# Kernel optimization log

Hardware: AMD Instinct MI355X
Metric: run time of the kernel (lower is better)

The kernel has to match this reference:

```python
import jax, jax.numpy as jnp
import numpy as np

N_HEAD = 12


def setup_inputs() -> dict:
    key = jax.random.key(0)
    kx, kq, kk, kv = jax.random.split(key, 4)
    b, n, d = 2, 2048, 768
    x = jax.random.normal(kx, (b, n, d), dtype=jnp.float32)
    # nn.Linear weights stored as [d_out, d_in]; y = x @ W.T (no bias, qkv_bias=False)
    scale = 1.0 / np.sqrt(d)
    Wq = jax.random.normal(kq, (d, d), dtype=jnp.float32) * scale
    Wk = jax.random.normal(kk, (d, d), dtype=jnp.float32) * scale
    Wv = jax.random.normal(kv, (d, d), dtype=jnp.float32) * scale
    return {"x": x, "Wq": Wq, "Wk": Wk, "Wv": Wv}


def reference(x, Wq, Wk, Wv):
    b, n, d = x.shape
    h = N_HEAD
    hd = d // h
    # linear projections (bias=False): x @ W.T, then split heads -> [b, h, n, hd]
    q = (x @ Wq.T).reshape(b, n, h, hd).transpose(0, 2, 1, 3)
    k = (x @ Wk.T).reshape(b, n, h, hd).transpose(0, 2, 1, 3)
    v = (x @ Wv.T).reshape(b, n, h, hd).transpose(0, 2, 1, 3)
    # raw (unscaled!) attention scores, matching the source (no / sqrt(head_dim))
    scores = jnp.einsum('bhqd,bhkd->bhqk', q, k)  # [b, h, n, n]
    causal = jnp.tril(jnp.ones((n, n), dtype=bool))
    scores = jnp.where(causal, scores, -jnp.inf)
    weights = jax.nn.softmax(scores, axis=-1)
    out = jnp.einsum('bhqk,bhkd->bhqd', weights, v)  # [b, h, n, hd]
    return out.transpose(0, 2, 1, 3).reshape(b, n, d)
```

## Files before the change

### kernel.cpp

```cpp
#include <hip/hip_runtime.h>
#include <hip/hip_bf16.h>
#include <stdint.h>

#define Bsz 2
#define NT  2048
#define DM  768
#define NH  12
#define HD  64
#define MT  (Bsz * NT)
#define NCAT (3 * DM)

typedef float    f32x4  __attribute__((ext_vector_type(4)));
typedef float    f32x16 __attribute__((ext_vector_type(16)));
typedef short    s16x8  __attribute__((ext_vector_type(8)));
typedef _Float16 f16x8  __attribute__((ext_vector_type(8)));
typedef int      v2i    __attribute__((ext_vector_type(2)));

#define GLOBAL_AS __attribute__((address_space(1)))
#define SHARED_AS __attribute__((address_space(3)))
#define LOG2E 1.44269504088896f

__device__ inline unsigned short f2h(float f) {
    union { _Float16 h; unsigned short u; } c; c.h = (_Float16)f; return c.u;
}
__device__ inline f16x8 ldh(const short* p) {
    return __builtin_bit_cast(f16x8, *(const s16x8*)p);
}
__device__ inline float exp2i(float x) {
    float r;
    asm("v_exp_f32 %0, %1" : "=v"(r) : "v"(x));
    return r;
}
__device__ inline int cvtpkh(float lo, float hi_) {
    int r;
    asm("v_cvt_pkrtz_f16_f32 %0, %1, %2" : "=v"(r) : "v"(lo), "v"(hi_));
    return r;
}
__device__ inline void plswap(int& a, int& b) {
    v2i r = __builtin_amdgcn_permlane32_swap(a, b, false, false);
    a = r[0]; b = r[1];
}
__device__ inline f16x8 mk8(int a, int b, int c, int d) {
    union { int i[4]; f16x8 v; } u;
    u.i[0] = a; u.i[1] = b; u.i[2] = c; u.i[3] = d;
    return u.v;
}
#define mfma32 __builtin_amdgcn_mfma_f32_32x32x16_f16
#define mfma16 __builtin_amdgcn_mfma_f32_16x16x32_f16


__global__ __launch_bounds__(256) void cvt_x_kernel(const float* __restrict__ x,
                                                    short* __restrict__ xf, int n8) {
    int i = blockIdx.x * blockDim.x + threadIdx.x;
    if (i >= n8) return;
    const float4* p = (const float4*)x + (size_t)i * 2;
    float4 a = p[0], b = p[1];
    float v[8] = {a.x, a.y, a.z, a.w, b.x, b.y, b.z, b.w};
    union { unsigned short s[8]; uint4 q; } H;
#pragma unroll
    for (int j = 0; j < 8; ++j) H.s[j] = f2h(v[j]);
    ((uint4*)xf)[i] = H.q;
}

__global__ __launch_bounds__(256) void cvt_w_kernel(const float* __restrict__ Wq,
                                                    const float* __restrict__ Wk,
                                                    const float* __restrict__ Wv,
                                                    short* __restrict__ Wf, int per8) {
    int i = blockIdx.x * blockDim.x + threadIdx.x;
    if (i >= 3 * per8) return;
    const float* src; int j;
    if (i < per8)          { src = Wq; j = i; }
    else if (i < 2 * per8) { src = Wk; j = i - per8; }
    else                   { src = Wv; j = i - 2 * per8; }
    const float4* p = (const float4*)src + (size_t)j * 2;
    float4 a = p[0], b = p[1];
    float v[8] = {a.x, a.y, a.z, a.w, b.x, b.y, b.z, b.w};
    union { unsigned short s[8]; uint4 q; } H;
#pragma unroll
    for (int t = 0; t < 8; ++t) H.s[t] = f2h(v[t]);
    ((uint4*)Wf)[i] = H.q;
}


#define BM 128
#define BK 32
#define KSTEPS (DM / BK)

__global__ __launch_bounds__(256, 2) void qkv_proj_kernel(
        const short* __restrict__ xf, const short* __restrict__ Wf,
        short* __restrict__ Qf, short* __restrict__ Kf, short* __restrict__ Vf) {
    __shared__ short lds[2][2][BM * BK];

    const int tid = threadIdx.x;
    const int w = tid >> 6, lane = tid & 63;
    const int l15 = lane & 15, lg = lane >> 4;
    const int wr = w >> 1, wc = w & 1;

    const int tile_m = blockIdx.x * BM;
    const int tile_n = blockIdx.y * BM;

    const int arr = w >> 1, hlf = w & 1;
    const int srow = lane >> 2;
    const int scol = (lane & 3) * 8;
    const short* gsrc = (arr == 0) ? xf + (size_t)tile_m * DM
                                   : Wf + (size_t)tile_n * DM;
    const short* gsrc_lane = gsrc + (size_t)(hlf * 64 + srow) * DM + scol;

    f32x4 zero4 = {0.f, 0.f, 0.f, 0.f};
    f32x4 acc[4][4];
#pragma unroll
    for (int i = 0; i < 4; ++i)
#pragma unroll
        for (int j = 0; j < 4; ++j) acc[i][j] = zero4;

    auto stage = [&](int buf, int kt) {
        const short* g = gsrc_lane + kt * BK;
#pragma unroll
        for (int j = 0; j < 4; ++j) {
            __builtin_amdgcn_global_load_lds(
                (const GLOBAL_AS void*)(g + (size_t)j * 16 * DM),
                (SHARED_AS void*)(&lds[buf][arr][(hlf * 64 + j * 16) * BK]),
                16, 0, 0);
        }
    };

    stage(0, 0);
    int cur = 0;
    for (int kt = 0; kt < KSTEPS; ++kt) {
        __syncthreads();
        if (kt + 1 < KSTEPS) stage(cur ^ 1, kt + 1);

        f16x8 a[4], b[4];
#pragma unroll
        for (int f = 0; f < 4; ++f) {
            a[f] = ldh(&lds[cur][0][(wr * 64 + f * 16 + l15) * BK + lg * 8]);
            b[f] = ldh(&lds[cur][1][(wc * 64 + f * 16 + l15) * BK + lg * 8]);
        }
#pragma unroll
        for (int mf = 0; mf < 4; ++mf)
#pragma unroll
            for (int nf = 0; nf < 4; ++nf)
                acc[mf][nf] = mfma16(a[mf], b[nf], acc[mf][nf], 0, 0, 0);
        cur ^= 1;
    }

    const int zq = tile_n / DM;
    const int ncol0 = tile_n % DM;
#pragma unroll
    for (int mf = 0; mf < 4; ++mf) {
#pragma unroll
        for (int nf = 0; nf < 4; ++nf) {
            int col = ncol0 + wc * 64 + nf * 16 + l15;
            int h = col >> 6, dh = col & 63;
            int m0 = tile_m + wr * 64 + mf * 16 + lg * 4;
            int b2 = m0 >> 11, nt0 = m0 & (NT - 1);
            int bh_ = b2 * NH + h;
            if (zq == 2) {
                union { short s[4]; short4 v; } pk;
#pragma unroll
                for (int r = 0; r < 4; ++r) pk.s[r] = (short)f2h(acc[mf][nf][r]);
                *(short4*)&Vf[((size_t)bh_ * HD + dh) * NT + nt0] = pk.v;
            } else {
                short* Hp = (zq == 0) ? Qf : Kf;
                float scl = (zq == 0) ? LOG2E : 1.0f;
#pragma unroll
                for (int r = 0; r < 4; ++r) {
                    size_t oidx = ((size_t)bh_ * NT + nt0 + r) * HD + dh;
                    Hp[oidx] = (short)f2h(acc[mf][nf][r] * scl);
                }
            }
        }
    }
}


#define QB  128
#define KVB 64
#define NQB (NT / QB)
#define SEGT 8
#define SLOTS 40
#define OPA 600

__global__ __launch_bounds__(256) void attn_part_kernel(const short* __restrict__ Qf,
                                                        const short* __restrict__ Kf,
                                                        const short* __restrict__ Vf,
                                                        short* __restrict__ OpA_,
                                                        short* __restrict__ OpB_,
                                                        float2* __restrict__ ml) {
    const int s = blockIdx.x;
    int qb, seg;
    if (s < 4)       { qb = s;                  seg = 0; }
    else if (s < 12) { qb = 4 + ((s - 4) >> 1);   seg = (s - 4) & 1; }
    else if (s < 24) { qb = 8 + (s - 12) / 3;     seg = (s - 12) % 3; }
    else             { qb = 12 + ((s - 24) >> 2); seg = (s - 24) & 3; }
    const int bh = blockIdx.y;
    const int g = bh * SLOTS + s;
    const int tid = threadIdx.x;
    const int w = tid >> 6, lane = tid & 63;
    const int l31 = lane & 31, hi = lane >> 5;

    __shared__ __align__(16) short lds[2][2 * 4096];

    const size_t kvoff = (size_t)bh * NT * HD;
    const short* Kfb = Kf + kvoff;
    const short* Vb  = Vf + (size_t)bh * HD * NT;

    const short* sbase[4]; int sstr[4]; int sdof[4];
#pragma unroll
    for (int k = 0; k < 4; ++k) {
        int c = tid + 256 * k;
        int arr = c >> 9, idx = c & 511;
        int row = idx >> 3, ch = idx & 7;
        if (arr == 0) { sbase[k] = Kfb + (size_t)row * HD + ch * 8; sstr[k] = KVB * HD; }
        else          { sbase[k] = Vb + (size_t)row * NT + ch * 8;  sstr[k] = KVB; }
        sdof[k] = arr * 4096 + row * 64 + ((ch ^ (row & 7)) << 3);
    }

    const int q0w   = qb * QB + w * 32;
    const int qg    = q0w + l31;
    const int qmaxw = q0w + 31;

    f16x8 qf[4];
    const size_t qrow = kvoff + (size_t)qg * HD;
#pragma unroll
    for (int c = 0; c < 4; ++c) qf[c] = ldh(Qf + qrow + c * 16 + hi * 8);

    f32x16 o0{}, o1{};
    float m_run = -1e30f, l_run = 0.f;

    const int t0   = seg * SEGT;
    const int tend = min(t0 + SEGT, 2 * qb + 2);

    {
        uint4 ld0[4];
#pragma unroll
        for (int k = 0; k < 4; ++k) ld0[k] = *(const uint4*)(sbase[k] + (size_t)t0 * sstr[k]);
#pragma unroll
        for (int k = 0; k < 4; ++k) *(uint4*)(&lds[0][sdof[k]]) = ld0[k];
    }

    for (int t = t0; t < tend; ++t) {
        __syncthreads();
        const int cur = (t - t0) & 1;
        const int kv0 = t * KVB;
        const bool haveNext = (t + 1 < tend);
        uint4 ldn[4];
        if (haveNext) {
#pragma unroll
            for (int k = 0; k < 4; ++k)
                ldn[k] = *(const uint4*)(sbase[k] + (size_t)(t + 1) * sstr[k]);
        }

        if (kv0 <= qmaxw) {
            const short* Ks = &lds[cur][0];
            const short* Vs = &lds[cur][4096];
            f32x16 Sa{}, Sb{};
            const int swbA = l31 * 64;
            const int swbB = (32 + l31) * 64;
            const int sw7  = l31 & 7;
#pragma unroll
            for (int c = 0; c < 4; ++c) {
                int sh = (((c << 1) + hi) ^ sw7) << 3;
                Sa = mfma32(ldh(&Ks[swbA + sh]), qf[c], Sa, 0, 0, 0);
                Sb = mfma32(ldh(&Ks[swbB + sh]), qf[c], Sb, 0, 0, 0);
            }
            const bool haveB = (kv0 + 32 <= qmaxw);
            float pmax = -3e38f;
            if (kv0 + 31 > q0w) {
#pragma unroll
                for (int r = 0; r < 16; ++r) {
                    int kvg = kv0 + (r & 3) + 8 * (r >> 2) + 4 * hi;
                    Sa[r] = (kvg > qg) ? -3e38f : Sa[r];
                    pmax = fmaxf(pmax, Sa[r]);
                }
            } else {
#pragma unroll
                for (int r = 0; r < 16; ++r) pmax = fmaxf(pmax, Sa[r]);
            }
            if (haveB) {
                if (kv0 + 63 > q0w) {
#pragma unroll
                    for (int r = 0; r < 16; ++r) {
                        int kvg = kv0 + 32 + (r & 3) + 8 * (r >> 2) + 4 * hi;
                        Sb[r] = (kvg > qg) ? -3e38f : Sb[r];
                        pmax = fmaxf(pmax, Sb[r]);
                    }
                } else {
#pragma unroll
                    for (int r = 0; r < 16; ++r) pmax = fmaxf(pmax, Sb[r]);
                }
            }
            pmax = fmaxf(pmax, __shfl_xor(pmax, 32));
            if (!__all(pmax - m_run <= 11.5416f)) {
                float mn = fmaxf(m_run, pmax);
                float al = exp2i(m_run - mn);
                m_run = mn; l_run *= al;
                int ai = __builtin_bit_cast(int, al);
#pragma unroll
                for (int r = 0; r < 16; ++r) {
                    int kr = (r & 3) + 8 * (r >> 2) + 4 * hi;
                    float av = __builtin_bit_cast(float,
                                  __builtin_amdgcn_ds_bpermute(kr << 2, ai));
                    o0[r] *= av; o1[r] *= av;
                }
            }
            float rs = 0.f;
#pragma unroll
            for (int r = 0; r < 16; ++r) { Sa[r] = exp2i(Sa[r] - m_run); rs += Sa[r]; }
            if (haveB) {
#pragma unroll
                for (int r = 0; r < 16; ++r) { Sb[r] = exp2i(Sb[r] - m_run); rs += Sb[r]; }
            }
            rs += __shfl_xor(rs, 32);
            l_run += rs;
            {
                int cpk[8];
#pragma unroll
                for (int i = 0; i < 8; ++i) cpk[i] = cvtpkh(Sa[2 * i], Sa[2 * i + 1]);
                int a0 = cpk[0], b0 = cpk[2]; plswap(a0, b0);
                int a1 = cpk[1], b1 = cpk[3]; plswap(a1, b1);
                int a2 = cpk[4], b2 = cpk[6]; plswap(a2, b2);
                int a3 = cpk[5], b3 = cpk[7]; plswap(a3, b3);
                f16x8 pf[2] = { mk8(a0, a1, b0, b1), mk8(a2, a3, b2, b3) };
#pragma unroll
                for (int kc = 0; kc < 2; ++kc) {
                    int chunk = kc * 2 + hi;
                    int sh = (chunk ^ (l31 & 7)) << 3;
                    o0 = mfma32(pf[kc], ldh(&Vs[l31 * 64 + sh]), o0, 0, 0, 0);
                    o1 = mfma32(pf[kc], ldh(&Vs[(32 + l31) * 64 + sh]), o1, 0, 0, 0);
                }
            }
            if (haveB) {
                int cpk[8];
#pragma unroll
                for (int i = 0; i < 8; ++i) cpk[i] = cvtpkh(Sb[2 * i], Sb[2 * i + 1]);
                int a0 = cpk[0], b0 = cpk[2]; plswap(a0, b0);
                int a1 = cpk[1], b1 = cpk[3]; plswap(a1, b1);
                int a2 = cpk[4], b2 = cpk[6]; plswap(a2, b2);
                int a3 = cpk[5], b3 = cpk[7]; plswap(a3, b3);
                f16x8 pf[2] = { mk8(a0, a1, b0, b1), mk8(a2, a3, b2, b3) };
#pragma unroll
                for (int kc = 0; kc < 2; ++kc) {
                    int chunk = 4 + kc * 2 + hi;
                    int sh = (chunk ^ (l31 & 7)) << 3;
                    o0 = mfma32(pf[kc], ldh(&Vs[l31 * 64 + sh]), o0, 0, 0, 0);
                    o1 = mfma32(pf[kc], ldh(&Vs[(32 + l31) * 64 + sh]), o1, 0, 0, 0);
                }
            }
        }

        if (haveNext) {
#pragma unroll
            for (int k = 0; k < 4; ++k) *(uint4*)(&lds[cur ^ 1][sdof[k]]) = ldn[k];
        }
    }

    float inv = 1.0f / l_run;
    int ii = __builtin_bit_cast(int, inv);
    short* op = (g < OPA) ? OpA_ + (size_t)g * (QB * HD)
                          : OpB_ + (size_t)(g - OPA) * (QB * HD);
#pragma unroll
    for (int r = 0; r < 16; ++r) {
        int kr = (r & 3) + 8 * (r >> 2) + 4 * hi;
        float iv = __builtin_bit_cast(float, __builtin_amdgcn_ds_bpermute(kr << 2, ii));
        short* orow = op + (w * 32 + kr) * HD;
        orow[l31]      = (short)f2h(o0[r] * iv);
        orow[32 + l31] = (short)f2h(o1[r] * iv);
    }
    if (hi == 0) {
        float2 v; v.x = m_run; v.y = l_run;
        ml[(size_t)g * QB + w * 32 + l31] = v;
    }
}


__global__ __launch_bounds__(256) void combine_kernel(const short* __restrict__ OpA_,
                                                      const short* __restrict__ OpB_,
                                                      const float2* __restrict__ ml,
                                                      float* __restrict__ out) {
    const int qb = blockIdx.x, bh = blockIdx.y;
    const int b = bh / NH, h = bh % NH;
    const int nseg = (qb >> 2) + 1;
    const int baseg[4] = {0, 4, 12, 24};
    const int sbase = baseg[qb >> 2] + (qb & 3) * nseg;
    const int row = threadIdx.x >> 1;
    const int c0 = (threadIdx.x & 1) * 32;

    float m[4], l[4];
    float M = -3e38f;
    for (int s2 = 0; s2 < nseg; ++s2) {
        float2 t = ml[((size_t)(bh * SLOTS + sbase + s2)) * QB + row];
        m[s2] = t.x; l[s2] = t.y;
        M = fmaxf(M, t.x);
    }
    float wgt[4], L = 0.f;
    for (int s2 = 0; s2 < nseg; ++s2) {
        float e;
        asm("v_exp_f32 %0, %1" : "=v"(e) : "v"(m[s2] - M));
        wgt[s2] = l[s2] * e; L += wgt[s2];
    }
    float invL = 1.0f / L;

    float acc[32];
#pragma unroll
    for (int j = 0; j < 32; ++j) acc[j] = 0.f;
    for (int s2 = 0; s2 < nseg; ++s2) {
        int g = bh * SLOTS + sbase + s2;
        const short* opg = (g < OPA) ? OpA_ + (size_t)g * (QB * HD)
                                     : OpB_ + (size_t)(g - OPA) * (QB * HD);
        const short* oprow = opg + (size_t)row * HD + c0;
        float wg = wgt[s2] * invL;
#pragma unroll
        for (int v = 0; v < 4; ++v) {
            f16x8 d = ldh(oprow + v * 8);
#pragma unroll
            for (int j = 0; j < 8; ++j)
                acc[v * 8 + j] += wg * (float)d[j];
        }
    }
    float* orow = out + ((size_t)(b * NT + qb * QB + row)) * DM + h * HD + c0;
#pragma unroll
    for (int j = 0; j < 32; ++j) orow[j] = acc[j];
}


extern "C" void kernel_launch(void* const* d_in, const int* in_sizes, int n_in,
                              void* d_out, int out_size, void* d_ws, size_t ws_size,
                              hipStream_t stream) {
    const float* x  = (const float*)d_in[0];
    const float* Wq = (const float*)d_in[1];
    const float* Wk = (const float*)d_in[2];
    const float* Wv = (const float*)d_in[3];
    float* outp = (float*)d_out;

    const size_t MD = (size_t)MT * DM;
    const size_t DD = (size_t)DM * DM;

    short* wsp = (short*)d_ws;
    short* xf = wsp;
    short* Wf = xf + MD;
    short* Qf = Wf + 3 * DD;
    short* Kf = Qf + MD;
    short* Vf = Kf + MD;
    short* OpA_ = wsp;
    short* OpB_ = Vf + MD;
    float2* mlp = (float2*)(OpB_ + (size_t)360 * QB * HD);

    int n8x = (int)(MD / 8);
    cvt_x_kernel<<<dim3((n8x + 255) / 256), 256, 0, stream>>>(x, xf, n8x);
    int per8 = (int)(DD / 8);
    cvt_w_kernel<<<dim3((3 * per8 + 255) / 256), 256, 0, stream>>>(Wq, Wk, Wv, Wf, per8);
    qkv_proj_kernel<<<dim3(MT / BM, NCAT / BM), 256, 0, stream>>>(xf, Wf, Qf, Kf, Vf);
    attn_part_kernel<<<dim3(SLOTS, Bsz * NH), 256, 0, stream>>>(Qf, Kf, Vf, OpA_, OpB_, mlp);
    combine_kernel<<<dim3(NQB, Bsz * NH), 256, 0, stream>>>(OpA_, OpB_, mlp, outp);
}
```

Baseline: 161.7 us.

## Load K/V tiles directly from global into registers, dropping LDS staging

```diff
diff --git a/kernel.cpp b/kernel.cpp
--- a/kernel.cpp
+++ b/kernel.cpp
@@ -199,22 +199,10 @@
     const int w = tid >> 6, lane = tid & 63;
     const int l31 = lane & 31, hi = lane >> 5;
 
-    __shared__ __align__(16) short lds[2][2 * 4096];
-
     const size_t kvoff = (size_t)bh * NT * HD;
-    const short* Kfb = Kf + kvoff;
-    const short* Vb  = Vf + (size_t)bh * HD * NT;
-
-    const short* sbase[4]; int sstr[4]; int sdof[4];
-#pragma unroll
-    for (int k = 0; k < 4; ++k) {
-        int c = tid + 256 * k;
-        int arr = c >> 9, idx = c & 511;
-        int row = idx >> 3, ch = idx & 7;
-        if (arr == 0) { sbase[k] = Kfb + (size_t)row * HD + ch * 8; sstr[k] = KVB * HD; }
-        else          { sbase[k] = Vb + (size_t)row * NT + ch * 8;  sstr[k] = KVB; }
-        sdof[k] = arr * 4096 + row * 64 + ((ch ^ (row & 7)) << 3);
-    }
+    const short* kbase = Kf + kvoff + (size_t)l31 * HD + hi * 8;
+    const short* vb0   = Vf + (size_t)bh * HD * NT + (size_t)l31 * NT + hi * 8;
+    const short* vb1   = vb0 + (size_t)32 * NT;
 
     const int q0w   = qb * QB + w * 32;
     const int qg    = q0w + l31;
@@ -228,130 +216,118 @@
     f32x16 o0{}, o1{};
     float m_run = -1e30f, l_run = 0.f;
 
-    const int t0   = seg * SEGT;
-    const int tend = min(t0 + SEGT, 2 * qb + 2);
-
-    {
-        uint4 ld0[4];
-#pragma unroll
-        for (int k = 0; k < 4; ++k) ld0[k] = *(const uint4*)(sbase[k] + (size_t)t0 * sstr[k]);
-#pragma unroll
-        for (int k = 0; k < 4; ++k) *(uint4*)(&lds[0][sdof[k]]) = ld0[k];
-    }
-
-    for (int t = t0; t < tend; ++t) {
-        __syncthreads();
-        const int cur = (t - t0) & 1;
+    const int t0    = seg * SEGT;
+    const int tendA = min(t0 + SEGT, 2 * qb + 2);
+    const int tendW = min(tendA, qmaxw / KVB + 1);
+
+    for (int t = t0; t < tendW; ++t) {
         const int kv0 = t * KVB;
-        const bool haveNext = (t + 1 < tend);
-        uint4 ldn[4];
-        if (haveNext) {
-#pragma unroll
-            for (int k = 0; k < 4; ++k)
-                ldn[k] = *(const uint4*)(sbase[k] + (size_t)(t + 1) * sstr[k]);
-        }
-
-        if (kv0 <= qmaxw) {
-            const short* Ks = &lds[cur][0];
-            const short* Vs = &lds[cur][4096];
-            f32x16 Sa{}, Sb{};
-            const int swbA = l31 * 64;
-            const int swbB = (32 + l31) * 64;
-            const int sw7  = l31 & 7;
-#pragma unroll
-            for (int c = 0; c < 4; ++c) {
-                int sh = (((c << 1) + hi) ^ sw7) << 3;
-                Sa = mfma32(ldh(&Ks[swbA + sh]), qf[c], Sa, 0, 0, 0);
-                Sb = mfma32(ldh(&Ks[swbB + sh]), qf[c], Sb, 0, 0, 0);
+        const bool haveB = (kv0 + 32 <= qmaxw);
+        const short* kt = kbase + (size_t)kv0 * HD;
+
+        f16x8 ka[4], kb[4];
+#pragma unroll
+        for (int c = 0; c < 4; ++c) ka[c] = ldh(kt + c * 16);
+        if (haveB) {
+#pragma unroll
+            for (int c = 0; c < 4; ++c) kb[c] = ldh(kt + 32 * HD + c * 16);
+        }
+
+        f32x16 Sa{}, Sb{};
+#pragma unroll
+        for (int c = 0; c < 4; ++c) Sa = mfma32(ka[c], qf[c], Sa, 0, 0, 0);
+        if (haveB) {
+#pragma unroll
+            for (int c = 0; c < 4; ++c) Sb = mfma32(kb[c], qf[c], Sb, 0, 0, 0);
+        }
+
+        f16x8 va[4], vbf[4];
+        const short* vt0 = vb0 + kv0;
+        const short* vt1 = vb1 + kv0;
+#pragma unroll
+        for (int j = 0; j < 4; ++j) {
+            int off = (j >> 1) * 32 + (j & 1) * 16;
+            va[j]  = ldh(vt0 + off);
+            vbf[j] = ldh(vt1 + off);
+        }
+
+        float pmax = -3e38f;
+        if (kv0 + 31 > q0w) {
+#pragma unroll
+            for (int r = 0; r < 16; ++r) {
+                int kvg = kv0 + (r & 3) + 8 * (r >> 2) + 4 * hi;
+                Sa[r] = (kvg > qg) ? -3e38f : Sa[r];
+                pmax = fmaxf(pmax, Sa[r]);
             }
-            const bool haveB = (kv0 + 32 <= qmaxw);
-            float pmax = -3e38f;
-            if (kv0 + 31 > q0w) {
+        } else {
+#pragma unroll
+            for (int r = 0; r < 16; ++r) pmax = fmaxf(pmax, Sa[r]);
+        }
+        if (haveB) {
+            if (kv0 + 63 > q0w) {
 #pragma unroll
                 for (int r = 0; r < 16; ++r) {
-                    int kvg = kv0 + (r & 3) + 8 * (r >> 2) + 4 * hi;
-                    Sa[r] = (kvg > qg) ? -3e38f : Sa[r];
-                    pmax = fmaxf(pmax, Sa[r]);
+                    int kvg = kv0 + 32 + (r & 3) + 8 * (r >> 2) + 4 * hi;
+                    Sb[r] = (kvg > qg) ? -3e38f : Sb[r];
+                    pmax = fmaxf(pmax, Sb[r]);
                 }
             } else {
 #pragma unroll
-                for (int r = 0; r < 16; ++r) pmax = fmaxf(pmax, Sa[r]);
+                for (int r = 0; r < 16; ++r) pmax = fmaxf(pmax, Sb[r]);
             }
-            if (haveB) {
-                if (kv0 + 63 > q0w) {
-#pragma unroll
-                    for (int r = 0; r < 16; ++r) {
-                        int kvg = kv0 + 32 + (r & 3) + 8 * (r >> 2) + 4 * hi;
-                        Sb[r] = (kvg > qg) ? -3e38f : Sb[r];
-                        pmax = fmaxf(pmax, Sb[r]);
-                    }
-                } else {
-#pragma unroll
-                    for (int r = 0; r < 16; ++r) pmax = fmaxf(pmax, Sb[r]);
-                }
+        }
+        pmax = fmaxf(pmax, __shfl_xor(pmax, 32));
+
+        if (!__all(pmax - m_run <= 11.5416f)) {
+            float mn = fmaxf(m_run, pmax);
+            float al = exp2i(m_run - mn);
+            m_run = mn; l_run *= al;
+            int ai = __builtin_bit_cast(int, al);
+#pragma unroll
+            for (int r = 0; r < 16; ++r) {
+                int kr = (r & 3) + 8 * (r >> 2) + 4 * hi;
+                float av = __builtin_bit_cast(float,
+                              __builtin_amdgcn_ds_bpermute(kr << 2, ai));
+                o0[r] *= av; o1[r] *= av;
             }
-            pmax = fmaxf(pmax, __shfl_xor(pmax, 32));
-            if (!__all(pmax - m_run <= 11.5416f)) {
-                float mn = fmaxf(m_run, pmax);
-                float al = exp2i(m_run - mn);
-                m_run = mn; l_run *= al;
-                int ai = __builtin_bit_cast(int, al);
-#pragma unroll
-                for (int r = 0; r < 16; ++r) {
-                    int kr = (r & 3) + 8 * (r >> 2) + 4 * hi;
-                    float av = __builtin_bit_cast(float,
-                                  __builtin_amdgcn_ds_bpermute(kr << 2, ai));
-                    o0[r] *= av; o1[r] *= av;
-                }
-            }
-            float rs = 0.f;
-#pragma unroll
-            for (int r = 0; r < 16; ++r) { Sa[r] = exp2i(Sa[r] - m_run); rs += Sa[r]; }
-            if (haveB) {
-#pragma unroll
-                for (int r = 0; r < 16; ++r) { Sb[r] = exp2i(Sb[r] - m_run); rs += Sb[r]; }
-            }
-            rs += __shfl_xor(rs, 32);
-            l_run += rs;
-            {
-                int cpk[8];
-#pragma unroll
-                for (int i = 0; i < 8; ++i) cpk[i] = cvtpkh(Sa[2 * i], Sa[2 * i + 1]);
-                int a0 = cpk[0], b0 = cpk[2]; plswap(a0, b0);
-                int a1 = cpk[1], b1 = cpk[3]; plswap(a1, b1);
-                int a2 = cpk[4], b2 = cpk[6]; plswap(a2, b2);
-                int a3 = cpk[5], b3 = cpk[7]; plswap(a3, b3);
-                f16x8 pf[2] = { mk8(a0, a1, b0, b1), mk8(a2, a3, b2, b3) };
-#pragma unroll
-                for (int kc = 0; kc < 2; ++kc) {
-                    int chunk = kc * 2 + hi;
-                    int sh = (chunk ^ (l31 & 7)) << 3;
-                    o0 = mfma32(pf[kc], ldh(&Vs[l31 * 64 + sh]), o0, 0, 0, 0);
-                    o1 = mfma32(pf[kc], ldh(&Vs[(32 + l31) * 64 + sh]), o1, 0, 0, 0);
-                }
-            }
-            if (haveB) {
-                int cpk[8];
-#pragma unroll
-                for (int i = 0; i < 8; ++i) cpk[i] = cvtpkh(Sb[2 * i], Sb[2 * i + 1]);
-                int a0 = cpk[0], b0 = cpk[2]; plswap(a0, b0);
-                int a1 = cpk[1], b1 = cpk[3]; plswap(a1, b1);
-                int a2 = cpk[4], b2 = cpk[6]; plswap(a2, b2);
-                int a3 = cpk[5], b3 = cpk[7]; plswap(a3, b3);
-                f16x8 pf[2] = { mk8(a0, a1, b0, b1), mk8(a2, a3, b2, b3) };
-#pragma unroll
-                for (int kc = 0; kc < 2; ++kc) {
-                    int chunk = 4 + kc * 2 + hi;
-                    int sh = (chunk ^ (l31 & 7)) << 3;
-                    o0 = mfma32(pf[kc], ldh(&Vs[l31 * 64 + sh]), o0, 0, 0, 0);
-                    o1 = mfma32(pf[kc], ldh(&Vs[(32 + l31) * 64 + sh]), o1, 0, 0, 0);
-                }
-            }
-        }
-
-        if (haveNext) {
-#pragma unroll
-            for (int k = 0; k < 4; ++k) *(uint4*)(&lds[cur ^ 1][sdof[k]]) = ldn[k];
+        }
+        float rs = 0.f;
+#pragma unroll
+        for (int r = 0; r < 16; ++r) { Sa[r] = exp2i(Sa[r] - m_run); rs += Sa[r]; }
+        if (haveB) {
+#pragma unroll
+            for (int r = 0; r < 16; ++r) { Sb[r] = exp2i(Sb[r] - m_run); rs += Sb[r]; }
+        }
+        rs += __shfl_xor(rs, 32);
+        l_run += rs;
+
+        {
+            int cpk[8];
+#pragma unroll
+            for (int i = 0; i < 8; ++i) cpk[i] = cvtpkh(Sa[2 * i], Sa[2 * i + 1]);
+            int a0 = cpk[0], b0 = cpk[2]; plswap(a0, b0);
+            int a1 = cpk[1], b1 = cpk[3]; plswap(a1, b1);
+            int a2 = cpk[4], b2 = cpk[6]; plswap(a2, b2);
+            int a3 = cpk[5], b3 = cpk[7]; plswap(a3, b3);
+            f16x8 pf[2] = { mk8(a0, a1, b0, b1), mk8(a2, a3, b2, b3) };
+            o0 = mfma32(pf[0], va[0], o0, 0, 0, 0);
+            o0 = mfma32(pf[1], va[1], o0, 0, 0, 0);
+            o1 = mfma32(pf[0], vbf[0], o1, 0, 0, 0);
+            o1 = mfma32(pf[1], vbf[1], o1, 0, 0, 0);
+        }
+        if (haveB) {
+            int cpk[8];
+#pragma unroll
+            for (int i = 0; i < 8; ++i) cpk[i] = cvtpkh(Sb[2 * i], Sb[2 * i + 1]);
+            int a0 = cpk[0], b0 = cpk[2]; plswap(a0, b0);
+            int a1 = cpk[1], b1 = cpk[3]; plswap(a1, b1);
+            int a2 = cpk[4], b2 = cpk[6]; plswap(a2, b2);
+            int a3 = cpk[5], b3 = cpk[7]; plswap(a3, b3);
+            f16x8 pf[2] = { mk8(a0, a1, b0, b1), mk8(a2, a3, b2, b3) };
+            o0 = mfma32(pf[0], va[2], o0, 0, 0, 0);
+            o0 = mfma32(pf[1], va[3], o0, 0, 0, 0);
+            o1 = mfma32(pf[0], vbf[2], o1, 0, 0, 0);
+            o1 = mfma32(pf[1], vbf[3], o1, 0, 0, 0);
         }
     }
 
```

Result: slower. 170.4 us (+5.4%).
